# Optimization experiments

Hardware: AMD Instinct MI355X
Metric: run time of the kernel (lower is better)

## Reference

```python
import jax, jax.numpy as jnp
import numpy as np

HEADS = 16
D_H = 64
ALPHA = 1.0


def _skew(QEr):
    # Music-Transformer skew: (b,h,n,n) -> relative-to-absolute
    b, h, i, j = QEr.shape
    pad = jnp.pad(QEr, ((0, 0), (0, 0), (0, 0), (1, 0)))  # (b,h,i,j+1)
    return pad.reshape(b, h, j + 1, i)[:, :, 1:, :]  # (b,h,i,j)


def _gather_bias(q, table, idx, heads):
    # q: (b,h,i,d); table: (S,d); idx: (b,i,j) int -> (b,h,i,j)
    b, h, i, d = q.shape
    QE = jnp.einsum('bhid,sd->bhis', q, table)  # (b,h,i,S)
    idx_b = jnp.broadcast_to(idx[:, None, :, :], (b, h, i, idx.shape[-1]))
    return jnp.take_along_axis(QE, idx_b, axis=-1)


def setup_inputs() -> dict:
    key = jax.random.key(0)
    ks = jax.random.split(key, 16)
    b, n, dim = 2, 1024, 1024
    d_h = dim // HEADS
    inp = {
        'x': jax.random.normal(ks[0], (b, n, dim), dtype=jnp.float32),
        'rel_bar': jax.random.randint(ks[1], (b, n, n), 0, 17, dtype=jnp.int32),
        'rel_position': jax.random.randint(ks[2], (b, n, n), 0, 96, dtype=jnp.int32),
        'rel_octave': jax.random.randint(ks[3], (b, n, n), 0, 25, dtype=jnp.int32),
        'rel_semitone': jax.random.randint(ks[4], (b, n, n), 0, 13, dtype=jnp.int32),
        'Wq': jax.random.normal(ks[5], (dim, dim), dtype=jnp.float32) * 0.02,
        'Wk': jax.random.normal(ks[6], (dim, dim), dtype=jnp.float32) * 0.02,
        'Wv': jax.random.normal(ks[7], (dim, dim), dtype=jnp.float32) * 0.02,
        'Wo': jax.random.normal(ks[8], (dim, dim), dtype=jnp.float32) * 0.02,
        'Er': jax.random.normal(ks[9], (n, d_h), dtype=jnp.float32),
        'Er_bar': jax.random.normal(ks[10], (16, d_h), dtype=jnp.float32),
        'Er_position': jax.random.normal(ks[11], (95, d_h), dtype=jnp.float32),
        'Er_octave': jax.random.normal(ks[12], (24, d_h), dtype=jnp.float32),
        'Er_semitone': jax.random.normal(ks[13], (12, d_h), dtype=jnp.float32),
    }
    return inp


def reference(x, rel_bar, rel_position, rel_octave, rel_semitone,
              Wq, Wk, Wv, Wo, Er, Er_bar, Er_position, Er_octave, Er_semitone):
    b, n, dim = x.shape
    h, d = HEADS, dim // HEADS

    def split_heads(t):
        return t.reshape(b, n, h, d).transpose(0, 2, 1, 3)  # (b,h,n,d)

    q = split_heads(x @ Wq.T)
    k = split_heads(x @ Wk.T)
    v = split_heads(x @ Wv.T)

    QK_t = jnp.einsum('bhid,bhjd->bhij', q, k)

    # relative-index bias (Music-Transformer style)
    QEr = jnp.einsum('bhid,jd->bhij', q, Er)  # start = max_seq_len - n = 0
    Srel = _skew(QEr)

    zrow = jnp.zeros((1, d), dtype=x.dtype)
    S_bar = _gather_bias(q, jnp.concatenate([Er_bar, zrow]), rel_bar, h)
    S_position = _gather_bias(q, jnp.concatenate([Er_position, zrow]), rel_position, h)
    S_octave = _gather_bias(q, jnp.concatenate([Er_octave, zrow]), rel_octave, h)
    S_semitone = _gather_bias(q, jnp.concatenate([Er_semitone, zrow]), rel_semitone, h)

    S_time = S_bar + S_position
    S_pitch = S_octave + S_semitone

    scores = (QK_t + Srel + ALPHA * (S_time + S_pitch)) / jnp.sqrt(jnp.asarray(d, x.dtype))
    causal = jnp.tril(jnp.ones((n, n), dtype=bool))
    scores = jnp.where(causal[None, None], scores, jnp.asarray(-1e9, x.dtype))
    attn = jax.nn.softmax(scores, axis=-1)

    out = jnp.einsum('bhij,bhjd->bhid', attn, v)
    out = out.transpose(0, 2, 1, 3).reshape(b, n, dim)
    return out @ Wo.T
```

## Files before the change

### kernel.cpp

```cpp
#include <hip/hip_runtime.h>


using bf16x8 = __attribute__((ext_vector_type(8))) short;
using f32x4  = __attribute__((ext_vector_type(4))) float;

__device__ __forceinline__ float bf2f(unsigned short u) {
  unsigned x = ((unsigned)u) << 16;
  float f;
  __builtin_memcpy(&f, &x, 4);
  return f;
}
__device__ __forceinline__ unsigned short f2bf(float f) {
  unsigned x;
  __builtin_memcpy(&x, &f, 4);
  unsigned r = (x + 0x7FFFu + ((x >> 16) & 1u)) >> 16;
  return (unsigned short)r;
}

union B8 { bf16x8 v; unsigned short u[8]; };

__global__ __launch_bounds__(256) void cast_all(
    const float* __restrict__ x,  const float* __restrict__ Wq,
    const float* __restrict__ Wk, const float* __restrict__ Wv,
    const float* __restrict__ Wo, const float* __restrict__ Er,
    unsigned short* __restrict__ x_bf, unsigned short* __restrict__ Wqkv,
    unsigned short* __restrict__ Wo_bf, unsigned short* __restrict__ Er_bf)
{
  const int total = 1589248;
  for (int i = blockIdx.x * 256 + threadIdx.x; i < total; i += gridDim.x * 256) {
    const float4* s4;
    ushort4* d4;
    if (i < 524288)       { s4 = (const float4*)x  + i;           d4 = (ushort4*)x_bf  + i; }
    else if (i < 786432)  { s4 = (const float4*)Wq + (i-524288);  d4 = (ushort4*)Wqkv  + (i-524288); }
    else if (i < 1048576) { s4 = (const float4*)Wk + (i-786432);  d4 = (ushort4*)Wqkv  + (i-786432) + 262144; }
    else if (i < 1310720) { s4 = (const float4*)Wv + (i-1048576); d4 = (ushort4*)Wqkv  + (i-1048576) + 524288; }
    else if (i < 1572864) { s4 = (const float4*)Wo + (i-1310720); d4 = (ushort4*)Wo_bf + (i-1310720); }
    else                  { s4 = (const float4*)Er + (i-1572864); d4 = (ushort4*)Er_bf + (i-1572864); }
    const float4 v = *s4;
    ushort4 o;
    o.x = f2bf(v.x); o.y = f2bf(v.y); o.z = f2bf(v.z); o.w = f2bf(v.w);
    *d4 = o;
  }
}

__global__ __launch_bounds__(256) void build_tpad(
    const float* __restrict__ Tb, const float* __restrict__ Tp,
    const float* __restrict__ To, const float* __restrict__ Ts,
    unsigned short* __restrict__ Tpad)
{
  const int t = blockIdx.x * 256 + threadIdx.x;
  if (t >= 10240) return;
  const int s = t >> 6, d = t & 63;
  float v = 0.f;
  if (s < 16)       v = Tb[s * 64 + d];
  else if (s == 16) v = 0.f;
  else if (s < 112) v = Tp[(s - 17) * 64 + d];
  else if (s < 113) v = 0.f;
  else if (s < 137) v = To[(s - 113) * 64 + d];
  else if (s < 138) v = 0.f;
  else if (s < 150) v = Ts[(s - 138) * 64 + d];
  Tpad[t] = f2bf(v * 0.125f);
}

__global__ __launch_bounds__(256) void pack_idx(
    const int* __restrict__ rb, const int* __restrict__ rp,
    const int* __restrict__ ro, const int* __restrict__ rs,
    unsigned* __restrict__ o, int n4)
{
  for (int i = blockIdx.x * 256 + threadIdx.x; i < n4; i += gridDim.x * 256) {
    const int4 a = ((const int4*)rb)[i];
    const int4 b = ((const int4*)rp)[i];
    const int4 c = ((const int4*)ro)[i];
    const int4 d = ((const int4*)rs)[i];
    uint4 r;
    r.x = (unsigned)(a.x | (17+b.x)<<5 | (113+c.x)<<12 | (138+d.x)<<20);
    r.y = (unsigned)(a.y | (17+b.y)<<5 | (113+c.y)<<12 | (138+d.y)<<20);
    r.z = (unsigned)(a.z | (17+b.z)<<5 | (113+c.z)<<12 | (138+d.z)<<20);
    r.w = (unsigned)(a.w | (17+b.w)<<5 | (113+c.w)<<12 | (138+d.w)<<20);
    ((uint4*)o)[i] = r;
  }
}

__device__ __forceinline__ void ld_lds16(const unsigned short* g, unsigned short* l) {
  __builtin_amdgcn_global_load_lds(
      (const __attribute__((address_space(1))) unsigned int*)g,
      (__attribute__((address_space(3))) unsigned int*)l, 16, 0, 0);
}

template <int MODE>
__global__ __launch_bounds__(256) void gemm128(const unsigned short* __restrict__ A,
                                               const unsigned short* __restrict__ B,
                                               void* __restrict__ Cv,
                                               int M, int N, int K)
{
  __shared__ __align__(16) unsigned short Atile[128 * 32];
  __shared__ __align__(16) unsigned short Btile[128 * 32];
  const int tid = threadIdx.x;
  const int w = tid >> 6, lane = tid & 63;
  const int c15 = lane & 15, q = lane >> 4;
  const int wr = w >> 1, wc = w & 1;
  const int n0 = blockIdx.x * 128, m0 = blockIdx.y * 128;

  const unsigned short* ag = A + (size_t)(m0 + (tid >> 2)) * K + (tid & 3) * 8;
  const unsigned short* bg = B + (size_t)(n0 + (tid >> 2)) * K + (tid & 3) * 8;
  unsigned short* al = &Atile[tid * 8];
  unsigned short* bl = &Btile[tid * 8];
  const size_t half = (size_t)64 * K;

  f32x4 acc[4][4];
  #pragma unroll
  for (int mt = 0; mt < 4; mt++)
    #pragma unroll
    for (int nt = 0; nt < 4; nt++) { acc[mt][nt][0]=0.f; acc[mt][nt][1]=0.f; acc[mt][nt][2]=0.f; acc[mt][nt][3]=0.f; }

  for (int k0 = 0; k0 < K; k0 += 32) {
    __syncthreads();
    ld_lds16(ag + k0, al);
    ld_lds16(ag + half + k0, al + 2048);
    ld_lds16(bg + k0, bl);
    ld_lds16(bg + half + k0, bl + 2048);
    __syncthreads();

    bf16x8 af[4], bfr[4];
    #pragma unroll
    for (int mt = 0; mt < 4; mt++)
      af[mt] = *(const bf16x8*)&Atile[(wr * 64 + mt * 16 + c15) * 32 + q * 8];
    #pragma unroll
    for (int nt = 0; nt < 4; nt++)
      bfr[nt] = *(const bf16x8*)&Btile[(wc * 64 + nt * 16 + c15) * 32 + q * 8];
    #pragma unroll
    for (int mt = 0; mt < 4; mt++)
      #pragma unroll
      for (int nt = 0; nt < 4; nt++)
        acc[mt][nt] = __builtin_amdgcn_mfma_f32_16x16x32_bf16(af[mt], bfr[nt], acc[mt][nt], 0, 0, 0);
  }

  #pragma unroll
  for (int mt = 0; mt < 4; mt++)
    #pragma unroll
    for (int nt = 0; nt < 4; nt++)
      #pragma unroll
      for (int r = 0; r < 4; r++) {
        const int m = m0 + wr * 64 + mt * 16 + q * 4 + r;
        const int n = n0 + wc * 64 + nt * 16 + c15;
        if constexpr (MODE == 1) {
          ((float*)Cv)[(size_t)m * N + n] = acc[mt][nt][r];
        } else {
          const int which = n >> 10, hh = (n >> 6) & 15, d = n & 63;
          const int bb = m >> 10, i = m & 1023;
          ((unsigned short*)Cv)[(size_t)which * 2097152 +
                                (((size_t)(bb << 4) + hh) << 16) + (i << 6) + d] = f2bf(acc[mt][nt][r]);
        }
      }
}

__global__ __launch_bounds__(256) void qe_gemm(const unsigned short* __restrict__ Qh,
                                               const unsigned short* __restrict__ Tpad,
                                               unsigned short* __restrict__ QE)
{
  __shared__ __align__(16) unsigned short T[160][72];
  const int tid = threadIdx.x;
  const int w = tid >> 6, lane = tid & 63;
  const int c15 = lane & 15, q = lane >> 4;
  const int m0 = blockIdx.x * 64 + w * 16;

  for (int t = tid; t < 1280; t += 256) {
    const int r = t >> 3, c = (t & 7) * 8;
    *(bf16x8*)&T[r][c] = *(const bf16x8*)(Tpad + r * 64 + c);
  }
  __syncthreads();

  bf16x8 a0, a1;
  {
    const unsigned short* ap = Qh + ((size_t)(m0 + c15) << 6) + q * 8;
    a0 = *(const bf16x8*)ap;
    a1 = *(const bf16x8*)(ap + 32);
  }
  unsigned short* out = QE + (size_t)m0 * 160;
  #pragma unroll
  for (int st = 0; st < 10; st++) {
    bf16x8 b0 = *(const bf16x8*)&T[st * 16 + c15][q * 8];
    bf16x8 b1 = *(const bf16x8*)&T[st * 16 + c15][32 + q * 8];
    f32x4 acc; acc[0]=0.f; acc[1]=0.f; acc[2]=0.f; acc[3]=0.f;
    acc = __builtin_amdgcn_mfma_f32_16x16x32_bf16(a0, b0, acc, 0, 0, 0);
    acc = __builtin_amdgcn_mfma_f32_16x16x32_bf16(a1, b1, acc, 0, 0, 0);
    #pragma unroll
    for (int r = 0; r < 4; r++) {
      const _Float16 hv = (_Float16)acc[r];
      unsigned short hb;
      __builtin_memcpy(&hb, &hv, 2);
      out[(size_t)(q * 4 + r) * 160 + st * 16 + c15] = hb;
    }
  }
}

__global__ __launch_bounds__(256) void attn_kernel(
    const unsigned short* __restrict__ QKVh,
    const unsigned short* __restrict__ QE,
    const unsigned* __restrict__ Pidx,
    const unsigned short* __restrict__ Er,
    unsigned short* __restrict__ Ob)
{
  const int h  = blockIdx.x;
  const int bb = blockIdx.z;
  const int it = bb ? (15 - (int)blockIdx.y) : (int)blockIdx.y;
  const int i0 = it << 6;
  const int tid = threadIdx.x;
  const int w = tid >> 6;
  const int lane = tid & 63;
  const int c15 = lane & 15;
  const int q = lane >> 4;
  const int rowq = q * 4;

  __shared__ __align__(16) unsigned short Klds[64][72];
  __shared__ __align__(16) unsigned short Vtlds[64][72];
  __shared__ __align__(16) unsigned short C2[4][16 * 88];
  __shared__ __align__(16) unsigned short qeh[64 * 160];
  unsigned short* c2w = &C2[w][0];

  const unsigned short* qhb = QKVh + (((size_t)(bb << 4) + h) << 16);
  const unsigned short* khb = qhb + 2097152;
  const unsigned short* vhb = qhb + 2 * 2097152;

  {
    const size_t qeoff = ((((size_t)(bb << 4) + h) * 1024) + i0) * 160;
    const unsigned short* src = QE + qeoff;
    for (int t = tid; t < 10240; t += 256) qeh[t] = src[t];
  }

  bf16x8 qf[2];
  {
    const unsigned short* qp = qhb + ((size_t)(i0 + w * 16 + c15) << 6);
    #pragma unroll
    for (int kk = 0; kk < 2; kk++) {
      B8 t;
      t.v = *(const bf16x8*)(qp + kk * 32 + q * 8);
      #pragma unroll
      for (int e = 0; e < 8; e++) t.u[e] = f2bf(bf2f(t.u[e]) * 0.125f);
      qf[kk] = t.v;
    }
  }

  f32x4 Oa[4];
  float mrow[4], lrow[4];
  #pragma unroll
  for (int dt = 0; dt < 4; dt++) { Oa[dt][0]=0.f; Oa[dt][1]=0.f; Oa[dt][2]=0.f; Oa[dt][3]=0.f; }
  #pragma unroll
  for (int r = 0; r < 4; r++) { mrow[r] = -3e38f; lrow[r] = 0.f; }

  const int iw = i0 + w * 16;
  const size_t idx0 = ((size_t)bb << 20) + ((size_t)(iw + rowq) << 10);

  for (int jt = 0; jt <= it; jt++) {
    const int j0 = jt << 6;
    __syncthreads();

    {
      const unsigned short* kt = khb + (j0 << 6);
      *(bf16x8*)&Klds[tid >> 3][(tid & 7) * 8]        = *(const bf16x8*)(kt + tid * 8);
      *(bf16x8*)&Klds[32 + (tid >> 3)][(tid & 7) * 8] = *(const bf16x8*)(kt + 2048 + tid * 8);
      const int vrow = tid >> 2, vcs = (tid & 3) * 16;
      const unsigned short* vt = vhb + (j0 << 6) + (vrow << 6) + vcs;
      B8 v0, v1;
      v0.v = *(const bf16x8*)vt;
      v1.v = *(const bf16x8*)(vt + 8);
      #pragma unroll
      for (int e = 0; e < 8; e++) {
        Vtlds[vcs + e][vrow]     = v0.u[e];
        Vtlds[vcs + 8 + e][vrow] = v1.u[e];
      }
    }
    __syncthreads();

    f32x4 S[4];
    #pragma unroll
    for (int nt = 0; nt < 4; nt++) {
      f32x4 a; a[0]=0.f; a[1]=0.f; a[2]=0.f; a[3]=0.f;
      bf16x8 k0 = *(const bf16x8*)&Klds[nt * 16 + c15][q * 8];
      bf16x8 k1 = *(const bf16x8*)&Klds[nt * 16 + c15][32 + q * 8];
      a = __builtin_amdgcn_mfma_f32_16x16x32_bf16(qf[0], k0, a, 0, 0, 0);
      a = __builtin_amdgcn_mfma_f32_16x16x32_bf16(qf[1], k1, a, 0, 0, 0);
      S[nt] = a;
    }

    {
      const int rbase = 960 - i0 + j0;
      #pragma unroll
      for (int t5 = 0; t5 < 5; t5++) {
        const int pt = 3 - w + t5;
        int row = rbase + pt * 16 + c15;
        row = row > 1023 ? 1023 : row;
        const unsigned short* ep = Er + (row << 6) + q * 8;
        bf16x8 e0 = *(const bf16x8*)ep;
        bf16x8 e1 = *(const bf16x8*)(ep + 32);
        f32x4 a; a[0]=0.f; a[1]=0.f; a[2]=0.f; a[3]=0.f;
        a = __builtin_amdgcn_mfma_f32_16x16x32_bf16(qf[0], e0, a, 0, 0, 0);
        a = __builtin_amdgcn_mfma_f32_16x16x32_bf16(qf[1], e1, a, 0, 0, 0);
        #pragma unroll
        for (int r = 0; r < 4; r++)
          c2w[(rowq + r) * 88 + t5 * 16 + c15] = f2bf(a[r]);
      }
    }

    #pragma unroll
    for (int nt = 0; nt < 4; nt++) {
      const int j = j0 + nt * 16 + c15;
      unsigned pv[4];
      #pragma unroll
      for (int r = 0; r < 4; r++)
        pv[r] = Pidx[idx0 + ((size_t)r << 10) + j];
      #pragma unroll
      for (int r = 0; r < 4; r++) {
        const int rb = (w * 16 + rowq + r) * 160;
        _Float16 q0, q1, q2, q3;
        __builtin_memcpy(&q0, &qeh[rb + (pv[r] & 31)], 2);
        __builtin_memcpy(&q1, &qeh[rb + ((pv[r] >> 5) & 127)], 2);
        __builtin_memcpy(&q2, &qeh[rb + ((pv[r] >> 12) & 255)], 2);
        __builtin_memcpy(&q3, &qeh[rb + (pv[r] >> 20)], 2);
        const float bias = (float)(q0 + q1) + (float)(q2 + q3);
        const float srel = bf2f(c2w[(rowq + r) * 88 + (15 - (rowq + r) + nt * 16 + c15)]);
        float sc = S[nt][r] + srel + bias;
        if (jt == it && j > iw + rowq + r) sc = -3e38f;
        S[nt][r] = sc;
      }
    }

    float alpha[4];
    #pragma unroll
    for (int r = 0; r < 4; r++) {
      float v = fmaxf(fmaxf(S[0][r], S[1][r]), fmaxf(S[2][r], S[3][r]));
      v = fmaxf(v, __shfl_xor(v, 1));
      v = fmaxf(v, __shfl_xor(v, 2));
      v = fmaxf(v, __shfl_xor(v, 4));
      v = fmaxf(v, __shfl_xor(v, 8));
      const float mn = fmaxf(mrow[r], v);
      alpha[r] = __expf(mrow[r] - mn);
      mrow[r] = mn;
    }
    #pragma unroll
    for (int nt = 0; nt < 4; nt++)
      #pragma unroll
      for (int r = 0; r < 4; r++)
        S[nt][r] = __expf(S[nt][r] - mrow[r]);
    #pragma unroll
    for (int r = 0; r < 4; r++) {
      float s = S[0][r] + S[1][r] + S[2][r] + S[3][r];
      s += __shfl_xor(s, 1);
      s += __shfl_xor(s, 2);
      s += __shfl_xor(s, 4);
      s += __shfl_xor(s, 8);
      lrow[r] = lrow[r] * alpha[r] + s;
      #pragma unroll
      for (int dt = 0; dt < 4; dt++) Oa[dt][r] *= alpha[r];
    }

    #pragma unroll
    for (int nt = 0; nt < 4; nt++)
      #pragma unroll
      for (int r = 0; r < 4; r++)
        c2w[(rowq + r) * 88 + nt * 16 + c15] = f2bf(S[nt][r]);

    bf16x8 pf[2];
    #pragma unroll
    for (int kk = 0; kk < 2; kk++)
      pf[kk] = *(const bf16x8*)&c2w[c15 * 88 + kk * 32 + q * 8];

    #pragma unroll
    for (int dt = 0; dt < 4; dt++) {
      bf16x8 v0 = *(const bf16x8*)&Vtlds[dt * 16 + c15][q * 8];
      bf16x8 v1 = *(const bf16x8*)&Vtlds[dt * 16 + c15][32 + q * 8];
      Oa[dt] = __builtin_amdgcn_mfma_f32_16x16x32_bf16(pf[0], v0, Oa[dt], 0, 0, 0);
      Oa[dt] = __builtin_amdgcn_mfma_f32_16x16x32_bf16(pf[1], v1, Oa[dt], 0, 0, 0);
    }
  }

  #pragma unroll
  for (int dt = 0; dt < 4; dt++)
    #pragma unroll
    for (int r = 0; r < 4; r++) {
      const int i_ = iw + rowq + r;
      const float o = Oa[dt][r] / lrow[r];
      Ob[(((size_t)bb << 10) + i_) * 1024 + (h << 6) + dt * 16 + c15] = f2bf(o);
    }
}

extern "C" void kernel_launch(void* const* d_in, const int* in_sizes, int n_in,
                              void* d_out, int out_size, void* d_ws, size_t ws_size,
                              hipStream_t stream)
{
  const float* x    = (const float*)d_in[0];
  const int*   rbar = (const int*)d_in[1];
  const int*   rpos = (const int*)d_in[2];
  const int*   roct = (const int*)d_in[3];
  const int*   rsem = (const int*)d_in[4];
  const float* Wq   = (const float*)d_in[5];
  const float* Wk   = (const float*)d_in[6];
  const float* Wv   = (const float*)d_in[7];
  const float* Wo   = (const float*)d_in[8];
  const float* Er   = (const float*)d_in[9];
  const float* Tb   = (const float*)d_in[10];
  const float* Tp   = (const float*)d_in[11];
  const float* To   = (const float*)d_in[12];
  const float* Ts   = (const float*)d_in[13];
  float* out = (float*)d_out;

  char* ws = (char*)d_ws;
  const size_t MB = 1u << 20;
  unsigned short* x_bf    = (unsigned short*)(ws);
  unsigned short* Wqkv_bf = (unsigned short*)(ws + 4 * MB);
  unsigned short* Wo_bf   = (unsigned short*)(ws + 10 * MB);
  unsigned short* Er_bf   = (unsigned short*)(ws + 12 * MB);
  unsigned short* Tpad    = (unsigned short*)(ws + 12 * MB + 256 * 1024);
  unsigned short* QKVh    = (unsigned short*)(ws + 13 * MB);
  unsigned short* Ob      = (unsigned short*)(ws + 25 * MB);
  unsigned short* QE      = (unsigned short*)(ws + 29 * MB);
  unsigned*       Pidx    = (unsigned*)(ws + 39 * MB);

  cast_all<<<1024, 256, 0, stream>>>(x, Wq, Wk, Wv, Wo, Er, x_bf, Wqkv_bf, Wo_bf, Er_bf);
  build_tpad<<<40, 256, 0, stream>>>(Tb, Tp, To, Ts, Tpad);
  pack_idx<<<1024, 256, 0, stream>>>(rbar, rpos, roct, rsem, Pidx, 524288);

  gemm128<2><<<dim3(24, 16), 256, 0, stream>>>(x_bf, Wqkv_bf, QKVh, 2048, 3072, 1024);
  qe_gemm<<<512, 256, 0, stream>>>(QKVh, Tpad, QE);
  attn_kernel<<<dim3(16, 16, 2), 256, 0, stream>>>(QKVh, QE, Pidx, Er_bf, Ob);
  gemm128<1><<<dim3(8, 16), 256, 0, stream>>>(Ob, Wo_bf, out, 2048, 1024, 1024);
}
```

Measured before the change: 269.9 us.

## Pre-transpose V globally, prefetch V and index loads, merge prep kernels

Merges the three preprocessing kernels into a single launch. Adds a separate kernel that transposes V into a global Vt buffer. The attention kernel then loads V fragments straight into registers instead of doing a scattered per-tile transpose through LDS. Pidx and V loads are issued before the barrier so they overlap with the K tile load, the QE tile copy is vectorised, and a minimum-occupancy launch bound is added. In exchange the code pays an extra kernel launch, an extra global round trip for V, and higher register pressure from the prefetched values.

```diff
diff --git a/kernel.cpp b/kernel.cpp
--- a/kernel.cpp
+++ b/kernel.cpp
@@ -19,65 +19,62 @@
 
 union B8 { bf16x8 v; unsigned short u[8]; };
 
-__global__ __launch_bounds__(256) void cast_all(
+__global__ __launch_bounds__(256) void prep(
     const float* __restrict__ x,  const float* __restrict__ Wq,
     const float* __restrict__ Wk, const float* __restrict__ Wv,
     const float* __restrict__ Wo, const float* __restrict__ Er,
-    unsigned short* __restrict__ x_bf, unsigned short* __restrict__ Wqkv,
-    unsigned short* __restrict__ Wo_bf, unsigned short* __restrict__ Er_bf)
-{
-  const int total = 1589248;
-  for (int i = blockIdx.x * 256 + threadIdx.x; i < total; i += gridDim.x * 256) {
-    const float4* s4;
-    ushort4* d4;
-    if (i < 524288)       { s4 = (const float4*)x  + i;           d4 = (ushort4*)x_bf  + i; }
-    else if (i < 786432)  { s4 = (const float4*)Wq + (i-524288);  d4 = (ushort4*)Wqkv  + (i-524288); }
-    else if (i < 1048576) { s4 = (const float4*)Wk + (i-786432);  d4 = (ushort4*)Wqkv  + (i-786432) + 262144; }
-    else if (i < 1310720) { s4 = (const float4*)Wv + (i-1048576); d4 = (ushort4*)Wqkv  + (i-1048576) + 524288; }
-    else if (i < 1572864) { s4 = (const float4*)Wo + (i-1310720); d4 = (ushort4*)Wo_bf + (i-1310720); }
-    else                  { s4 = (const float4*)Er + (i-1572864); d4 = (ushort4*)Er_bf + (i-1572864); }
-    const float4 v = *s4;
-    ushort4 o;
-    o.x = f2bf(v.x); o.y = f2bf(v.y); o.z = f2bf(v.z); o.w = f2bf(v.w);
-    *d4 = o;
-  }
-}
-
-__global__ __launch_bounds__(256) void build_tpad(
+    const int* __restrict__ rb, const int* __restrict__ rp,
+    const int* __restrict__ ro, const int* __restrict__ rs,
     const float* __restrict__ Tb, const float* __restrict__ Tp,
     const float* __restrict__ To, const float* __restrict__ Ts,
-    unsigned short* __restrict__ Tpad)
-{
-  const int t = blockIdx.x * 256 + threadIdx.x;
-  if (t >= 10240) return;
-  const int s = t >> 6, d = t & 63;
-  float v = 0.f;
-  if (s < 16)       v = Tb[s * 64 + d];
-  else if (s == 16) v = 0.f;
-  else if (s < 112) v = Tp[(s - 17) * 64 + d];
-  else if (s < 113) v = 0.f;
-  else if (s < 137) v = To[(s - 113) * 64 + d];
-  else if (s < 138) v = 0.f;
-  else if (s < 150) v = Ts[(s - 138) * 64 + d];
-  Tpad[t] = f2bf(v * 0.125f);
-}
-
-__global__ __launch_bounds__(256) void pack_idx(
-    const int* __restrict__ rb, const int* __restrict__ rp,
-    const int* __restrict__ ro, const int* __restrict__ rs,
-    unsigned* __restrict__ o, int n4)
-{
-  for (int i = blockIdx.x * 256 + threadIdx.x; i < n4; i += gridDim.x * 256) {
-    const int4 a = ((const int4*)rb)[i];
-    const int4 b = ((const int4*)rp)[i];
-    const int4 c = ((const int4*)ro)[i];
-    const int4 d = ((const int4*)rs)[i];
-    uint4 r;
-    r.x = (unsigned)(a.x | (17+b.x)<<5 | (113+c.x)<<12 | (138+d.x)<<20);
-    r.y = (unsigned)(a.y | (17+b.y)<<5 | (113+c.y)<<12 | (138+d.y)<<20);
-    r.z = (unsigned)(a.z | (17+b.z)<<5 | (113+c.z)<<12 | (138+d.z)<<20);
-    r.w = (unsigned)(a.w | (17+b.w)<<5 | (113+c.w)<<12 | (138+d.w)<<20);
-    ((uint4*)o)[i] = r;
+    unsigned short* __restrict__ x_bf, unsigned short* __restrict__ Wqkv,
+    unsigned short* __restrict__ Wo_bf, unsigned short* __restrict__ Er_bf,
+    unsigned* __restrict__ Pidx, unsigned short* __restrict__ Tpad)
+{
+  const int bid = blockIdx.x;
+  const int tid = threadIdx.x;
+  if (bid < 1024) {
+    const int total = 1589248;
+    for (int i = bid * 256 + tid; i < total; i += 1024 * 256) {
+      const float4* s4;
+      ushort4* d4;
+      if (i < 524288)       { s4 = (const float4*)x  + i;           d4 = (ushort4*)x_bf  + i; }
+      else if (i < 786432)  { s4 = (const float4*)Wq + (i-524288);  d4 = (ushort4*)Wqkv  + (i-524288); }
+      else if (i < 1048576) { s4 = (const float4*)Wk + (i-786432);  d4 = (ushort4*)Wqkv  + (i-786432) + 262144; }
+      else if (i < 1310720) { s4 = (const float4*)Wv + (i-1048576); d4 = (ushort4*)Wqkv  + (i-1048576) + 524288; }
+      else if (i < 1572864) { s4 = (const float4*)Wo + (i-1310720); d4 = (ushort4*)Wo_bf + (i-1310720); }
+      else                  { s4 = (const float4*)Er + (i-1572864); d4 = (ushort4*)Er_bf + (i-1572864); }
+      const float4 v = *s4;
+      ushort4 o;
+      o.x = f2bf(v.x); o.y = f2bf(v.y); o.z = f2bf(v.z); o.w = f2bf(v.w);
+      *d4 = o;
+    }
+  } else if (bid < 2048) {
+    for (int i = (bid - 1024) * 256 + tid; i < 524288; i += 1024 * 256) {
+      const int4 a = ((const int4*)rb)[i];
+      const int4 b = ((const int4*)rp)[i];
+      const int4 c = ((const int4*)ro)[i];
+      const int4 d = ((const int4*)rs)[i];
+      uint4 r;
+      r.x = (unsigned)(a.x | (17+b.x)<<5 | (113+c.x)<<12 | (138+d.x)<<20);
+      r.y = (unsigned)(a.y | (17+b.y)<<5 | (113+c.y)<<12 | (138+d.y)<<20);
+      r.z = (unsigned)(a.z | (17+b.z)<<5 | (113+c.z)<<12 | (138+d.z)<<20);
+      r.w = (unsigned)(a.w | (17+b.w)<<5 | (113+c.w)<<12 | (138+d.w)<<20);
+      ((uint4*)Pidx)[i] = r;
+    }
+  } else {
+    for (int t = tid; t < 10240; t += 256) {
+      const int s = t >> 6, d = t & 63;
+      float v = 0.f;
+      if (s < 16)       v = Tb[s * 64 + d];
+      else if (s == 16) v = 0.f;
+      else if (s < 112) v = Tp[(s - 17) * 64 + d];
+      else if (s < 113) v = 0.f;
+      else if (s < 137) v = To[(s - 113) * 64 + d];
+      else if (s < 138) v = 0.f;
+      else if (s < 150) v = Ts[(s - 138) * 64 + d];
+      Tpad[t] = f2bf(v * 0.125f);
+    }
   }
 }
 
@@ -154,6 +151,26 @@
       }
 }
 
+__global__ __launch_bounds__(256) void transpose_v(const unsigned short* __restrict__ V,
+                                                   unsigned short* __restrict__ Vt)
+{
+  __shared__ unsigned short T[64][72];
+  const int bh = blockIdx.x >> 4;
+  const int i0 = (blockIdx.x & 15) << 6;
+  const int tid = threadIdx.x;
+  const int row = tid >> 2, cs = (tid & 3) * 16;
+  const unsigned short* src = V + ((size_t)bh << 16) + ((size_t)(i0 + row) << 6) + cs;
+  *(bf16x8*)&T[row][cs]     = *(const bf16x8*)src;
+  *(bf16x8*)&T[row][cs + 8] = *(const bf16x8*)(src + 8);
+  __syncthreads();
+  B8 o0, o1;
+  #pragma unroll
+  for (int e = 0; e < 8; e++) { o0.u[e] = T[cs + e][row]; o1.u[e] = T[cs + 8 + e][row]; }
+  unsigned short* dst = Vt + ((size_t)bh << 16) + ((size_t)row << 10) + i0 + cs;
+  *(bf16x8*)dst       = o0.v;
+  *(bf16x8*)(dst + 8) = o1.v;
+}
+
 __global__ __launch_bounds__(256) void qe_gemm(const unsigned short* __restrict__ Qh,
                                                const unsigned short* __restrict__ Tpad,
                                                unsigned short* __restrict__ QE)
@@ -194,8 +211,9 @@
   }
 }
 
-__global__ __launch_bounds__(256) void attn_kernel(
+__global__ __launch_bounds__(256, 4) void attn_kernel(
     const unsigned short* __restrict__ QKVh,
+    const unsigned short* __restrict__ Vt,
     const unsigned short* __restrict__ QE,
     const unsigned* __restrict__ Pidx,
     const unsigned short* __restrict__ Er,
@@ -213,19 +231,19 @@
   const int rowq = q * 4;
 
   __shared__ __align__(16) unsigned short Klds[64][72];
-  __shared__ __align__(16) unsigned short Vtlds[64][72];
   __shared__ __align__(16) unsigned short C2[4][16 * 88];
   __shared__ __align__(16) unsigned short qeh[64 * 160];
   unsigned short* c2w = &C2[w][0];
 
-  const unsigned short* qhb = QKVh + (((size_t)(bb << 4) + h) << 16);
-  const unsigned short* khb = qhb + 2097152;
-  const unsigned short* vhb = qhb + 2 * 2097152;
+  const unsigned short* qhb  = QKVh + (((size_t)(bb << 4) + h) << 16);
+  const unsigned short* khb  = qhb + 2097152;
+  const unsigned short* vthb = Vt + (((size_t)(bb << 4) + h) << 16);
 
   {
     const size_t qeoff = ((((size_t)(bb << 4) + h) * 1024) + i0) * 160;
     const unsigned short* src = QE + qeoff;
-    for (int t = tid; t < 10240; t += 256) qeh[t] = src[t];
+    for (int t = tid; t < 1280; t += 256)
+      *(bf16x8*)&qeh[t * 8] = *(const bf16x8*)(src + t * 8);
   }
 
   bf16x8 qf[2];
@@ -253,22 +271,27 @@
 
   for (int jt = 0; jt <= it; jt++) {
     const int j0 = jt << 6;
+
+    unsigned pv[4][4];
+    #pragma unroll
+    for (int nt = 0; nt < 4; nt++)
+      #pragma unroll
+      for (int r = 0; r < 4; r++)
+        pv[nt][r] = Pidx[idx0 + ((size_t)r << 10) + j0 + nt * 16 + c15];
+    bf16x8 vf[4][2];
+    #pragma unroll
+    for (int dt = 0; dt < 4; dt++) {
+      const unsigned short* vp = vthb + ((size_t)(dt * 16 + c15) << 10) + j0 + q * 8;
+      vf[dt][0] = *(const bf16x8*)vp;
+      vf[dt][1] = *(const bf16x8*)(vp + 32);
+    }
+
     __syncthreads();
 
     {
       const unsigned short* kt = khb + (j0 << 6);
       *(bf16x8*)&Klds[tid >> 3][(tid & 7) * 8]        = *(const bf16x8*)(kt + tid * 8);
       *(bf16x8*)&Klds[32 + (tid >> 3)][(tid & 7) * 8] = *(const bf16x8*)(kt + 2048 + tid * 8);
-      const int vrow = tid >> 2, vcs = (tid & 3) * 16;
-      const unsigned short* vt = vhb + (j0 << 6) + (vrow << 6) + vcs;
-      B8 v0, v1;
-      v0.v = *(const bf16x8*)vt;
-      v1.v = *(const bf16x8*)(vt + 8);
-      #pragma unroll
-      for (int e = 0; e < 8; e++) {
-        Vtlds[vcs + e][vrow]     = v0.u[e];
-        Vtlds[vcs + 8 + e][vrow] = v1.u[e];
-      }
     }
     __syncthreads();
 
@@ -305,18 +328,15 @@
     #pragma unroll
     for (int nt = 0; nt < 4; nt++) {
       const int j = j0 + nt * 16 + c15;
-      unsigned pv[4];
-      #pragma unroll
-      for (int r = 0; r < 4; r++)
-        pv[r] = Pidx[idx0 + ((size_t)r << 10) + j];
       #pragma unroll
       for (int r = 0; r < 4; r++) {
         const int rb = (w * 16 + rowq + r) * 160;
+        const unsigned p = pv[nt][r];
         _Float16 q0, q1, q2, q3;
-        __builtin_memcpy(&q0, &qeh[rb + (pv[r] & 31)], 2);
-        __builtin_memcpy(&q1, &qeh[rb + ((pv[r] >> 5) & 127)], 2);
-        __builtin_memcpy(&q2, &qeh[rb + ((pv[r] >> 12) & 255)], 2);
-        __builtin_memcpy(&q3, &qeh[rb + (pv[r] >> 20)], 2);
+        __builtin_memcpy(&q0, &qeh[rb + (p & 31)], 2);
+        __builtin_memcpy(&q1, &qeh[rb + ((p >> 5) & 127)], 2);
+        __builtin_memcpy(&q2, &qeh[rb + ((p >> 12) & 255)], 2);
+        __builtin_memcpy(&q3, &qeh[rb + (p >> 20)], 2);
         const float bias = (float)(q0 + q1) + (float)(q2 + q3);
         const float srel = bf2f(c2w[(rowq + r) * 88 + (15 - (rowq + r) + nt * 16 + c15)]);
         float sc = S[nt][r] + srel + bias;
@@ -367,10 +387,8 @@
 
     #pragma unroll
     for (int dt = 0; dt < 4; dt++) {
-      bf16x8 v0 = *(const bf16x8*)&Vtlds[dt * 16 + c15][q * 8];
-      bf16x8 v1 = *(const bf16x8*)&Vtlds[dt * 16 + c15][32 + q * 8];
-      Oa[dt] = __builtin_amdgcn_mfma_f32_16x16x32_bf16(pf[0], v0, Oa[dt], 0, 0, 0);
-      Oa[dt] = __builtin_amdgcn_mfma_f32_16x16x32_bf16(pf[1], v1, Oa[dt], 0, 0, 0);
+      Oa[dt] = __builtin_amdgcn_mfma_f32_16x16x32_bf16(pf[0], vf[dt][0], Oa[dt], 0, 0, 0);
+      Oa[dt] = __builtin_amdgcn_mfma_f32_16x16x32_bf16(pf[1], vf[dt][1], Oa[dt], 0, 0, 0);
     }
   }
 
@@ -407,6 +425,7 @@
   char* ws = (char*)d_ws;
   const size_t MB = 1u << 20;
   unsigned short* x_bf    = (unsigned short*)(ws);
+  unsigned short* Vt      = (unsigned short*)(ws);
   unsigned short* Wqkv_bf = (unsigned short*)(ws + 4 * MB);
   unsigned short* Wo_bf   = (unsigned short*)(ws + 10 * MB);
   unsigned short* Er_bf   = (unsigned short*)(ws + 12 * MB);
@@ -416,12 +435,13 @@
   unsigned short* QE      = (unsigned short*)(ws + 29 * MB);
   unsigned*       Pidx    = (unsigned*)(ws + 39 * MB);
 
-  cast_all<<<1024, 256, 0, stream>>>(x, Wq, Wk, Wv, Wo, Er, x_bf, Wqkv_bf, Wo_bf, Er_bf);
-  build_tpad<<<40, 256, 0, stream>>>(Tb, Tp, To, Ts, Tpad);
-  pack_idx<<<1024, 256, 0, stream>>>(rbar, rpos, roct, rsem, Pidx, 524288);
+  prep<<<2049, 256, 0, stream>>>(x, Wq, Wk, Wv, Wo, Er, rbar, rpos, roct, rsem,
+                                 Tb, Tp, To, Ts,
+                                 x_bf, Wqkv_bf, Wo_bf, Er_bf, Pidx, Tpad);
 
   gemm128<2><<<dim3(24, 16), 256, 0, stream>>>(x_bf, Wqkv_bf, QKVh, 2048, 3072, 1024);
+  transpose_v<<<512, 256, 0, stream>>>(QKVh + 2 * 2097152, Vt);
   qe_gemm<<<512, 256, 0, stream>>>(QKVh, Tpad, QE);
-  attn_kernel<<<dim3(16, 16, 2), 256, 0, stream>>>(QKVh, QE, Pidx, Er_bf, Ob);
+  attn_kernel<<<dim3(16, 16, 2), 256, 0, stream>>>(QKVh, Vt, QE, Pidx, Er_bf, Ob);
   gemm128<1><<<dim3(8, 16), 256, 0, stream>>>(Ob, Wo_bf, out, 2048, 1024, 1024);
 }
```

Measured after the change: 301.0 us. 1.12x slower.

## Double-buffer K tiles with async LDS loads and merge prep kernels

Applied to the files above, without the earlier changes.

The attention kernel now prefetches the next K tile straight into a second LDS buffer using global_load_lds while the current tile is being processed. The barrier after tile loads is dropped and a single barrier is placed just before the P/V stage. Pidx loads are hoisted to the top of each iteration and the QE tile copy into LDS is vectorized. The three preprocessing kernels are merged into one launch to cut launch overhead. In exchange the kernel uses more LDS, and correctness now depends on the barriers also waiting for the async LDS loads to land.

```diff
diff --git a/kernel.cpp b/kernel.cpp
--- a/kernel.cpp
+++ b/kernel.cpp
@@ -19,65 +19,62 @@
 
 union B8 { bf16x8 v; unsigned short u[8]; };
 
-__global__ __launch_bounds__(256) void cast_all(
+__global__ __launch_bounds__(256) void prep(
     const float* __restrict__ x,  const float* __restrict__ Wq,
     const float* __restrict__ Wk, const float* __restrict__ Wv,
     const float* __restrict__ Wo, const float* __restrict__ Er,
-    unsigned short* __restrict__ x_bf, unsigned short* __restrict__ Wqkv,
-    unsigned short* __restrict__ Wo_bf, unsigned short* __restrict__ Er_bf)
-{
-  const int total = 1589248;
-  for (int i = blockIdx.x * 256 + threadIdx.x; i < total; i += gridDim.x * 256) {
-    const float4* s4;
-    ushort4* d4;
-    if (i < 524288)       { s4 = (const float4*)x  + i;           d4 = (ushort4*)x_bf  + i; }
-    else if (i < 786432)  { s4 = (const float4*)Wq + (i-524288);  d4 = (ushort4*)Wqkv  + (i-524288); }
-    else if (i < 1048576) { s4 = (const float4*)Wk + (i-786432);  d4 = (ushort4*)Wqkv  + (i-786432) + 262144; }
-    else if (i < 1310720) { s4 = (const float4*)Wv + (i-1048576); d4 = (ushort4*)Wqkv  + (i-1048576) + 524288; }
-    else if (i < 1572864) { s4 = (const float4*)Wo + (i-1310720); d4 = (ushort4*)Wo_bf + (i-1310720); }
-    else                  { s4 = (const float4*)Er + (i-1572864); d4 = (ushort4*)Er_bf + (i-1572864); }
-    const float4 v = *s4;
-    ushort4 o;
-    o.x = f2bf(v.x); o.y = f2bf(v.y); o.z = f2bf(v.z); o.w = f2bf(v.w);
-    *d4 = o;
-  }
-}
-
-__global__ __launch_bounds__(256) void build_tpad(
+    const int* __restrict__ rb, const int* __restrict__ rp,
+    const int* __restrict__ ro, const int* __restrict__ rs,
     const float* __restrict__ Tb, const float* __restrict__ Tp,
     const float* __restrict__ To, const float* __restrict__ Ts,
-    unsigned short* __restrict__ Tpad)
+    unsigned short* __restrict__ x_bf, unsigned short* __restrict__ Wqkv,
+    unsigned short* __restrict__ Wo_bf, unsigned short* __restrict__ Er_bf,
+    unsigned* __restrict__ Pidx, unsigned short* __restrict__ Tpad)
 {
-  const int t = blockIdx.x * 256 + threadIdx.x;
-  if (t >= 10240) return;
-  const int s = t >> 6, d = t & 63;
-  float v = 0.f;
-  if (s < 16)       v = Tb[s * 64 + d];
-  else if (s == 16) v = 0.f;
-  else if (s < 112) v = Tp[(s - 17) * 64 + d];
-  else if (s < 113) v = 0.f;
-  else if (s < 137) v = To[(s - 113) * 64 + d];
-  else if (s < 138) v = 0.f;
-  else if (s < 150) v = Ts[(s - 138) * 64 + d];
-  Tpad[t] = f2bf(v * 0.125f);
-}
-
-__global__ __launch_bounds__(256) void pack_idx(
-    const int* __restrict__ rb, const int* __restrict__ rp,
-    const int* __restrict__ ro, const int* __restrict__ rs,
-    unsigned* __restrict__ o, int n4)
-{
-  for (int i = blockIdx.x * 256 + threadIdx.x; i < n4; i += gridDim.x * 256) {
-    const int4 a = ((const int4*)rb)[i];
-    const int4 b = ((const int4*)rp)[i];
-    const int4 c = ((const int4*)ro)[i];
-    const int4 d = ((const int4*)rs)[i];
-    uint4 r;
-    r.x = (unsigned)(a.x | (17+b.x)<<5 | (113+c.x)<<12 | (138+d.x)<<20);
-    r.y = (unsigned)(a.y | (17+b.y)<<5 | (113+c.y)<<12 | (138+d.y)<<20);
-    r.z = (unsigned)(a.z | (17+b.z)<<5 | (113+c.z)<<12 | (138+d.z)<<20);
-    r.w = (unsigned)(a.w | (17+b.w)<<5 | (113+c.w)<<12 | (138+d.w)<<20);
-    ((uint4*)o)[i] = r;
+  const int bid = blockIdx.x;
+  const int tid = threadIdx.x;
+  if (bid < 1024) {
+    const int total = 1589248;
+    for (int i = bid * 256 + tid; i < total; i += 1024 * 256) {
+      const float4* s4;
+      ushort4* d4;
+      if (i < 524288)       { s4 = (const float4*)x  + i;           d4 = (ushort4*)x_bf  + i; }
+      else if (i < 786432)  { s4 = (const float4*)Wq + (i-524288);  d4 = (ushort4*)Wqkv  + (i-524288); }
+      else if (i < 1048576) { s4 = (const float4*)Wk + (i-786432);  d4 = (ushort4*)Wqkv  + (i-786432) + 262144; }
+      else if (i < 1310720) { s4 = (const float4*)Wv + (i-1048576); d4 = (ushort4*)Wqkv  + (i-1048576) + 524288; }
+      else if (i < 1572864) { s4 = (const float4*)Wo + (i-1310720); d4 = (ushort4*)Wo_bf + (i-1310720); }
+      else                  { s4 = (const float4*)Er + (i-1572864); d4 = (ushort4*)Er_bf + (i-1572864); }
+      const float4 v = *s4;
+      ushort4 o;
+      o.x = f2bf(v.x); o.y = f2bf(v.y); o.z = f2bf(v.z); o.w = f2bf(v.w);
+      *d4 = o;
+    }
+  } else if (bid < 2048) {
+    for (int i = (bid - 1024) * 256 + tid; i < 524288; i += 1024 * 256) {
+      const int4 a = ((const int4*)rb)[i];
+      const int4 b = ((const int4*)rp)[i];
+      const int4 c = ((const int4*)ro)[i];
+      const int4 d = ((const int4*)rs)[i];
+      uint4 r;
+      r.x = (unsigned)(a.x | (17+b.x)<<5 | (113+c.x)<<12 | (138+d.x)<<20);
+      r.y = (unsigned)(a.y | (17+b.y)<<5 | (113+c.y)<<12 | (138+d.y)<<20);
+      r.z = (unsigned)(a.z | (17+b.z)<<5 | (113+c.z)<<12 | (138+d.z)<<20);
+      r.w = (unsigned)(a.w | (17+b.w)<<5 | (113+c.w)<<12 | (138+d.w)<<20);
+      ((uint4*)Pidx)[i] = r;
+    }
+  } else {
+    for (int t = tid; t < 10240; t += 256) {
+      const int s = t >> 6, d = t & 63;
+      float v = 0.f;
+      if (s < 16)       v = Tb[s * 64 + d];
+      else if (s == 16) v = 0.f;
+      else if (s < 112) v = Tp[(s - 17) * 64 + d];
+      else if (s < 113) v = 0.f;
+      else if (s < 137) v = To[(s - 113) * 64 + d];
+      else if (s < 138) v = 0.f;
+      else if (s < 150) v = Ts[(s - 138) * 64 + d];
+      Tpad[t] = f2bf(v * 0.125f);
+    }
   }
 }
 
@@ -212,7 +209,7 @@
   const int q = lane >> 4;
   const int rowq = q * 4;
 
-  __shared__ __align__(16) unsigned short Klds[64][72];
+  __shared__ __align__(16) unsigned short Klds[2][64 * 64];
   __shared__ __align__(16) unsigned short Vtlds[64][72];
   __shared__ __align__(16) unsigned short C2[4][16 * 88];
   __shared__ __align__(16) unsigned short qeh[64 * 160];
@@ -222,10 +219,14 @@
   const unsigned short* khb = qhb + 2097152;
   const unsigned short* vhb = qhb + 2 * 2097152;
 
+  ld_lds16(khb + tid * 8,        &Klds[0][tid * 8]);
+  ld_lds16(khb + 2048 + tid * 8, &Klds[0][2048 + tid * 8]);
+
   {
     const size_t qeoff = ((((size_t)(bb << 4) + h) * 1024) + i0) * 160;
     const unsigned short* src = QE + qeoff;
-    for (int t = tid; t < 10240; t += 256) qeh[t] = src[t];
+    for (int t = tid; t < 1280; t += 256)
+      *(bf16x8*)&qeh[t * 8] = *(const bf16x8*)(src + t * 8);
   }
 
   bf16x8 qf[2];
@@ -253,12 +254,24 @@
 
   for (int jt = 0; jt <= it; jt++) {
     const int j0 = jt << 6;
+    const int cur = jt & 1;
+
     __syncthreads();
 
+    if (jt < it) {
+      const unsigned short* kn = khb + ((jt + 1) << 12);
+      ld_lds16(kn + tid * 8,        &Klds[cur ^ 1][tid * 8]);
+      ld_lds16(kn + 2048 + tid * 8, &Klds[cur ^ 1][2048 + tid * 8]);
+    }
+
+    unsigned pv[4][4];
+    #pragma unroll
+    for (int nt = 0; nt < 4; nt++)
+      #pragma unroll
+      for (int r = 0; r < 4; r++)
+        pv[nt][r] = Pidx[idx0 + ((size_t)r << 10) + j0 + nt * 16 + c15];
+
     {
-      const unsigned short* kt = khb + (j0 << 6);
-      *(bf16x8*)&Klds[tid >> 3][(tid & 7) * 8]        = *(const bf16x8*)(kt + tid * 8);
-      *(bf16x8*)&Klds[32 + (tid >> 3)][(tid & 7) * 8] = *(const bf16x8*)(kt + 2048 + tid * 8);
       const int vrow = tid >> 2, vcs = (tid & 3) * 16;
       const unsigned short* vt = vhb + (j0 << 6) + (vrow << 6) + vcs;
       B8 v0, v1;
@@ -270,14 +283,13 @@
         Vtlds[vcs + 8 + e][vrow] = v1.u[e];
       }
     }
-    __syncthreads();
 
     f32x4 S[4];
     #pragma unroll
     for (int nt = 0; nt < 4; nt++) {
       f32x4 a; a[0]=0.f; a[1]=0.f; a[2]=0.f; a[3]=0.f;
-      bf16x8 k0 = *(const bf16x8*)&Klds[nt * 16 + c15][q * 8];
-      bf16x8 k1 = *(const bf16x8*)&Klds[nt * 16 + c15][32 + q * 8];
+      bf16x8 k0 = *(const bf16x8*)&Klds[cur][(nt * 16 + c15) * 64 + q * 8];
+      bf16x8 k1 = *(const bf16x8*)&Klds[cur][(nt * 16 + c15) * 64 + 32 + q * 8];
       a = __builtin_amdgcn_mfma_f32_16x16x32_bf16(qf[0], k0, a, 0, 0, 0);
       a = __builtin_amdgcn_mfma_f32_16x16x32_bf16(qf[1], k1, a, 0, 0, 0);
       S[nt] = a;
@@ -305,18 +317,15 @@
     #pragma unroll
     for (int nt = 0; nt < 4; nt++) {
       const int j = j0 + nt * 16 + c15;
-      unsigned pv[4];
-      #pragma unroll
-      for (int r = 0; r < 4; r++)
-        pv[r] = Pidx[idx0 + ((size_t)r << 10) + j];
       #pragma unroll
       for (int r = 0; r < 4; r++) {
         const int rb = (w * 16 + rowq + r) * 160;
+        const unsigned p = pv[nt][r];
         _Float16 q0, q1, q2, q3;
-        __builtin_memcpy(&q0, &qeh[rb + (pv[r] & 31)], 2);
-        __builtin_memcpy(&q1, &qeh[rb + ((pv[r] >> 5) & 127)], 2);
-        __builtin_memcpy(&q2, &qeh[rb + ((pv[r] >> 12) & 255)], 2);
-        __builtin_memcpy(&q3, &qeh[rb + (pv[r] >> 20)], 2);
+        __builtin_memcpy(&q0, &qeh[rb + (p & 31)], 2);
+        __builtin_memcpy(&q1, &qeh[rb + ((p >> 5) & 127)], 2);
+        __builtin_memcpy(&q2, &qeh[rb + ((p >> 12) & 255)], 2);
+        __builtin_memcpy(&q3, &qeh[rb + (p >> 20)], 2);
         const float bias = (float)(q0 + q1) + (float)(q2 + q3);
         const float srel = bf2f(c2w[(rowq + r) * 88 + (15 - (rowq + r) + nt * 16 + c15)]);
         float sc = S[nt][r] + srel + bias;
@@ -353,6 +362,8 @@
       #pragma unroll
       for (int dt = 0; dt < 4; dt++) Oa[dt][r] *= alpha[r];
     }
+
+    __syncthreads();
 
     #pragma unroll
     for (int nt = 0; nt < 4; nt++)
@@ -416,9 +427,9 @@
   unsigned short* QE      = (unsigned short*)(ws + 29 * MB);
   unsigned*       Pidx    = (unsigned*)(ws + 39 * MB);
 
-  cast_all<<<1024, 256, 0, stream>>>(x, Wq, Wk, Wv, Wo, Er, x_bf, Wqkv_bf, Wo_bf, Er_bf);
-  build_tpad<<<40, 256, 0, stream>>>(Tb, Tp, To, Ts, Tpad);
-  pack_idx<<<1024, 256, 0, stream>>>(rbar, rpos, roct, rsem, Pidx, 524288);
+  prep<<<2049, 256, 0, stream>>>(x, Wq, Wk, Wv, Wo, Er, rbar, rpos, roct, rsem,
+                                 Tb, Tp, To, Ts,
+                                 x_bf, Wqkv_bf, Wo_bf, Er_bf, Pidx, Tpad);
 
   gemm128<2><<<dim3(24, 16), 256, 0, stream>>>(x_bf, Wqkv_bf, QKVh, 2048, 3072, 1024);
   qe_gemm<<<512, 256, 0, stream>>>(QKVh, Tpad, QE);
```

Result: faster. 252.8 us (-6.3%).
